# Performance work log

Hardware: AMD Instinct MI355X
Metric: run time of the kernel (lower is better)

## Reference

```python
import jax, jax.numpy as jnp
import numpy as np

N_NODES = 100000
N_EDGES = 1600000
N_FEAT = 256
HIDDEN = 128
N_CLASSES = 40


def gcn_conv(x, edge_index, W, b, num_nodes):
    # h = X W  (transform first, like torch_geometric GCNConv)
    h = x @ W  # [N, out]
    # add self loops
    loops = jnp.arange(num_nodes, dtype=edge_index.dtype)
    src = jnp.concatenate([edge_index[0], loops])
    dst = jnp.concatenate([edge_index[1], loops])
    # symmetric normalization: deg computed on dst (in-degree incl. self loop)
    deg = jax.ops.segment_sum(jnp.ones_like(dst, dtype=h.dtype), dst,
                              num_segments=num_nodes)
    dinv = jnp.where(deg > 0, jax.lax.rsqrt(deg), 0.0)
    norm = dinv[src] * dinv[dst]  # [E+N]
    # gather -> scale -> scatter-add
    msgs = h[src] * norm[:, None]
    out = jax.ops.segment_sum(msgs, dst, num_segments=num_nodes)
    return out + b


def setup_inputs() -> dict:
    key = jax.random.key(0)
    k1, k2, k3, k4, k5 = jax.random.split(key, 5)
    x = jax.random.normal(k1, (N_NODES, N_FEAT), dtype=jnp.float32)
    edge_index = jax.random.randint(k2, (2, N_EDGES), 0, N_NODES, dtype=jnp.int64)
    W1 = jax.random.normal(k3, (N_FEAT, HIDDEN), dtype=jnp.float32) * (1.0 / np.sqrt(N_FEAT))
    b1 = jnp.zeros((HIDDEN,), dtype=jnp.float32)
    W2 = jax.random.normal(k4, (HIDDEN, N_CLASSES), dtype=jnp.float32) * (1.0 / np.sqrt(HIDDEN))
    b2 = jnp.zeros((N_CLASSES,), dtype=jnp.float32)
    return {"x": x, "edge_index": edge_index, "W1": W1, "b1": b1, "W2": W2, "b2": b2}


def reference(x, edge_index, W1, b1, W2, b2):
    num_nodes = x.shape[0]
    h = gcn_conv(x, edge_index, W1, b1, num_nodes)
    h = jax.nn.relu(h)
    # dropout p=0.1 is identity in eval mode (self.training == False)
    out = gcn_conv(h, edge_index, W2, b2, num_nodes)
    return out
```

## Files before the change

### kernel.cpp

```cpp
#include <hip/hip_runtime.h>


#define NFEAT 256
#define HID   128
#define NCLS  40

__global__ void k_hist(const int* __restrict__ dst, int* __restrict__ deg, int E) {
    int stride = gridDim.x * blockDim.x;
    for (int e = blockIdx.x * blockDim.x + threadIdx.x; e < E; e += stride)
        atomicAdd(&deg[dst[e]], 1);
}

__global__ void k_scan1(const int* __restrict__ deg, int* __restrict__ rowptr,
                        int* __restrict__ blockSums, float* __restrict__ dinv, int N) {
    __shared__ int sums[256];
    int t = threadIdx.x;
    int base = blockIdx.x * 1024 + t * 4;
    int c[4];
#pragma unroll
    for (int j = 0; j < 4; j++) {
        int idx = base + j;
        c[j] = (idx < N) ? deg[idx] : 0;
        if (idx < N) dinv[idx] = rsqrtf((float)(c[j] + 1));
    }
    int s = c[0] + c[1] + c[2] + c[3];
    sums[t] = s;
    __syncthreads();
    for (int off = 1; off < 256; off <<= 1) {
        int v = (t >= off) ? sums[t - off] : 0;
        __syncthreads();
        sums[t] += v;
        __syncthreads();
    }
    int run = sums[t] - s;
#pragma unroll
    for (int j = 0; j < 4; j++) {
        int idx = base + j;
        if (idx < N) rowptr[idx] = run;
        run += c[j];
    }
    if (t == 255) blockSums[blockIdx.x] = sums[255];
}

__global__ void k_scan2(int* __restrict__ blockSums, int* __restrict__ rowptr,
                        int nblocks, int N) {
    __shared__ int sh[128];
    int t = threadIdx.x;
    int v = (t < nblocks) ? blockSums[t] : 0;
    sh[t] = v;
    __syncthreads();
    for (int off = 1; off < 128; off <<= 1) {
        int u = (t >= off) ? sh[t - off] : 0;
        __syncthreads();
        sh[t] += u;
        __syncthreads();
    }
    blockSums[t] = sh[t] - v;
    if (t == 127) rowptr[N] = sh[127];
}

__global__ void k_scan3(int* __restrict__ rowptr, const int* __restrict__ blockSums,
                        int* __restrict__ cursor, int N) {
    int stride = gridDim.x * blockDim.x;
    for (int i = blockIdx.x * blockDim.x + threadIdx.x; i < N; i += stride) {
        int v = rowptr[i] + blockSums[i >> 10];
        rowptr[i] = v;
        cursor[i] = v;
    }
}

__global__ void k_fill(const int* __restrict__ src, const int* __restrict__ dst,
                       int* __restrict__ cursor, int* __restrict__ col, int E) {
    int stride = gridDim.x * blockDim.x;
    for (int e = blockIdx.x * blockDim.x + threadIdx.x; e < E; e += stride) {
        int d = dst[e];
        int pos = atomicAdd(&cursor[d], 1);
        col[pos] = src[e];
    }
}

__global__ __launch_bounds__(256) void k_gemm1(const float* __restrict__ X,
                                               const float* __restrict__ W,
                                               const float* __restrict__ dinv,
                                               float* __restrict__ H, int M) {
    __shared__ float As[32][132];
    __shared__ float Bs[32][128];
    int t = threadIdx.x;
    int tx = t & 15, ty = t >> 4;
    int row0 = blockIdx.x * 128;

    float acc[8][8];
#pragma unroll
    for (int i = 0; i < 8; i++)
#pragma unroll
        for (int j = 0; j < 8; j++) acc[i][j] = 0.f;

    int arow = t >> 3;
    int acol = (t & 7) * 4;
    int brow = t >> 5;
    int bcol = (t & 31) * 4;

    for (int k0 = 0; k0 < NFEAT; k0 += 32) {
#pragma unroll
        for (int p = 0; p < 4; p++) {
            int r = p * 32 + arow;
            int gr = row0 + r;
            float4 v = make_float4(0.f, 0.f, 0.f, 0.f);
            if (gr < M) v = *(const float4*)&X[(size_t)gr * NFEAT + k0 + acol];
            As[acol + 0][r] = v.x; As[acol + 1][r] = v.y;
            As[acol + 2][r] = v.z; As[acol + 3][r] = v.w;
        }
#pragma unroll
        for (int p = 0; p < 4; p++) {
            int kr = p * 8 + brow;
            *(float4*)&Bs[kr][bcol] = *(const float4*)&W[(size_t)(k0 + kr) * HID + bcol];
        }
        __syncthreads();
#pragma unroll
        for (int kk = 0; kk < 32; kk++) {
            float a[8], b[8];
            *(float4*)&a[0] = *(const float4*)&As[kk][ty * 8];
            *(float4*)&a[4] = *(const float4*)&As[kk][ty * 8 + 4];
            *(float4*)&b[0] = *(const float4*)&Bs[kk][tx * 4];
            *(float4*)&b[4] = *(const float4*)&Bs[kk][64 + tx * 4];
#pragma unroll
            for (int i = 0; i < 8; i++)
#pragma unroll
                for (int j = 0; j < 8; j++) acc[i][j] += a[i] * b[j];
        }
        __syncthreads();
    }
#pragma unroll
    for (int i = 0; i < 8; i++) {
        int gr = row0 + ty * 8 + i;
        if (gr < M) {
            float dv = dinv[gr];
            float4 v0 = make_float4(acc[i][0] * dv, acc[i][1] * dv, acc[i][2] * dv, acc[i][3] * dv);
            float4 v1 = make_float4(acc[i][4] * dv, acc[i][5] * dv, acc[i][6] * dv, acc[i][7] * dv);
            *(float4*)&H[(size_t)gr * HID + tx * 4] = v0;
            *(float4*)&H[(size_t)gr * HID + 64 + tx * 4] = v1;
        }
    }
}

__global__ __launch_bounds__(256) void k_agg1(const float* __restrict__ H1,
                                              const int* __restrict__ rowptr,
                                              const int* __restrict__ col,
                                              const float* __restrict__ dinv,
                                              const float* __restrict__ b1,
                                              float* __restrict__ out, int N) {
    int node = blockIdx.x * 4 + (threadIdx.x >> 6);
    if (node >= N) return;
    int lane = threadIdx.x & 63;
    int g = lane >> 5;
    int c = lane & 31;

    float4 acc = make_float4(0.f, 0.f, 0.f, 0.f);
    if (g == 0)
        acc = *(const float4*)&H1[(size_t)node * HID + c * 4];

    int e = rowptr[node], e1 = rowptr[node + 1];
    for (; e + 7 < e1; e += 8) {
        int s0 = col[e + g];
        int s1 = col[e + 2 + g];
        int s2 = col[e + 4 + g];
        int s3 = col[e + 6 + g];
        float4 v0 = *(const float4*)&H1[(size_t)s0 * HID + c * 4];
        float4 v1 = *(const float4*)&H1[(size_t)s1 * HID + c * 4];
        float4 v2 = *(const float4*)&H1[(size_t)s2 * HID + c * 4];
        float4 v3 = *(const float4*)&H1[(size_t)s3 * HID + c * 4];
        acc.x += (v0.x + v1.x) + (v2.x + v3.x);
        acc.y += (v0.y + v1.y) + (v2.y + v3.y);
        acc.z += (v0.z + v1.z) + (v2.z + v3.z);
        acc.w += (v0.w + v1.w) + (v2.w + v3.w);
    }
    for (; e + 1 < e1; e += 2) {
        int s = col[e + g];
        float4 v = *(const float4*)&H1[(size_t)s * HID + c * 4];
        acc.x += v.x; acc.y += v.y; acc.z += v.z; acc.w += v.w;
    }
    if (e < e1 && g == 0) {
        int s = col[e];
        float4 v = *(const float4*)&H1[(size_t)s * HID + c * 4];
        acc.x += v.x; acc.y += v.y; acc.z += v.z; acc.w += v.w;
    }
    acc.x += __shfl_xor(acc.x, 32);
    acc.y += __shfl_xor(acc.y, 32);
    acc.z += __shfl_xor(acc.z, 32);
    acc.w += __shfl_xor(acc.w, 32);

    if (g == 0) {
        float dv = dinv[node];
        float4 bb = *(const float4*)&b1[c * 4];
        float4 r;
        r.x = fmaxf(acc.x * dv + bb.x, 0.f);
        r.y = fmaxf(acc.y * dv + bb.y, 0.f);
        r.z = fmaxf(acc.z * dv + bb.z, 0.f);
        r.w = fmaxf(acc.w * dv + bb.w, 0.f);
        *(float4*)&out[(size_t)node * HID + c * 4] = r;
    }
}

__global__ __launch_bounds__(256) void k_gemm2(const float* __restrict__ A,
                                               const float* __restrict__ W,
                                               const float* __restrict__ dinv,
                                               float* __restrict__ H, int M) {
    __shared__ float As[64][129];
    __shared__ float Ws[HID * NCLS];
    int t = threadIdx.x;
    for (int idx = t; idx < HID * NCLS; idx += 256) Ws[idx] = W[idx];

    int row0 = blockIdx.x * 64;
#pragma unroll
    for (int p = 0; p < 8; p++) {
        int flat = (p * 256 + t) * 4;
        int r = flat >> 7;
        int c = flat & 127;
        int gr = row0 + r;
        float4 v = make_float4(0.f, 0.f, 0.f, 0.f);
        if (gr < M) v = *(const float4*)&A[(size_t)gr * HID + c];
        As[r][c + 0] = v.x; As[r][c + 1] = v.y; As[r][c + 2] = v.z; As[r][c + 3] = v.w;
    }
    __syncthreads();

    int r = t >> 2;
    int cg = (t & 3) * 10;
    float acc[10];
#pragma unroll
    for (int j = 0; j < 10; j++) acc[j] = 0.f;
    for (int k = 0; k < HID; k++) {
        float a = As[r][k];
        const float* wrow = &Ws[k * NCLS + cg];
#pragma unroll
        for (int j = 0; j < 10; j++) acc[j] += a * wrow[j];
    }
    int gr = row0 + r;
    if (gr < M) {
        float dv = dinv[gr];
#pragma unroll
        for (int j = 0; j < 10; j++) H[(size_t)gr * NCLS + cg + j] = acc[j] * dv;
    }
}

__global__ __launch_bounds__(256) void k_agg2(const float* __restrict__ H2,
                                              const int* __restrict__ rowptr,
                                              const int* __restrict__ col,
                                              const float* __restrict__ dinv,
                                              const float* __restrict__ b2,
                                              float* __restrict__ out, int N) {
    int node = blockIdx.x * 4 + (threadIdx.x >> 6);
    if (node >= N) return;
    int lane = threadIdx.x & 63;
    int g = lane / 10;
    int c = lane % 10;
    bool active = g < 6;

    float4 acc = make_float4(0.f, 0.f, 0.f, 0.f);
    if (g == 0)
        acc = *(const float4*)&H2[(size_t)node * NCLS + c * 4];

    int e = rowptr[node], e1 = rowptr[node + 1];
    for (; e + 11 < e1; e += 12) {
        if (active) {
            int s0 = col[e + g];
            int s1 = col[e + 6 + g];
            float4 v0 = *(const float4*)&H2[(size_t)s0 * NCLS + c * 4];
            float4 v1 = *(const float4*)&H2[(size_t)s1 * NCLS + c * 4];
            acc.x += v0.x + v1.x;
            acc.y += v0.y + v1.y;
            acc.z += v0.z + v1.z;
            acc.w += v0.w + v1.w;
        }
    }
    for (; e < e1; e += 6) {
        int idx = e + g;
        if (active && idx < e1) {
            int s = col[idx];
            float4 v = *(const float4*)&H2[(size_t)s * NCLS + c * 4];
            acc.x += v.x; acc.y += v.y; acc.z += v.z; acc.w += v.w;
        }
    }
    float4 t1, t2;
    t1.x = __shfl(acc.x, lane + 30); t1.y = __shfl(acc.y, lane + 30);
    t1.z = __shfl(acc.z, lane + 30); t1.w = __shfl(acc.w, lane + 30);
    acc.x += t1.x; acc.y += t1.y; acc.z += t1.z; acc.w += t1.w;
    t1.x = __shfl(acc.x, lane + 10); t1.y = __shfl(acc.y, lane + 10);
    t1.z = __shfl(acc.z, lane + 10); t1.w = __shfl(acc.w, lane + 10);
    t2.x = __shfl(acc.x, lane + 20); t2.y = __shfl(acc.y, lane + 20);
    t2.z = __shfl(acc.z, lane + 20); t2.w = __shfl(acc.w, lane + 20);
    acc.x += t1.x + t2.x; acc.y += t1.y + t2.y;
    acc.z += t1.z + t2.z; acc.w += t1.w + t2.w;

    if (g == 0) {
        float dv = dinv[node];
        float4 bb = *(const float4*)&b2[c * 4];
        float4 r;
        r.x = acc.x * dv + bb.x;
        r.y = acc.y * dv + bb.y;
        r.z = acc.z * dv + bb.z;
        r.w = acc.w * dv + bb.w;
        *(float4*)&out[(size_t)node * NCLS + c * 4] = r;
    }
}

extern "C" void kernel_launch(void* const* d_in, const int* in_sizes, int n_in,
                              void* d_out, int out_size, void* d_ws, size_t ws_size,
                              hipStream_t stream) {
    const float* x  = (const float*)d_in[0];
    const int*   ei = (const int*)d_in[1];
    const float* W1 = (const float*)d_in[2];
    const float* b1 = (const float*)d_in[3];
    const float* W2 = (const float*)d_in[4];
    const float* b2 = (const float*)d_in[5];
    float* out = (float*)d_out;

    const int N = in_sizes[0] / NFEAT;
    const int E = in_sizes[1] / 2;
    const int* src = ei;
    const int* dst = ei + E;

    char* ws = (char*)d_ws;
    size_t off = 0;
    auto alloc = [&](size_t bytes) { size_t cur = off; off = (off + bytes + 255) & ~255ULL; return cur; };
    int*   deg       = (int*)(ws + alloc((size_t)N * 4));
    int*   rowptr    = (int*)(ws + alloc(((size_t)N + 1) * 4));
    int*   cursor    = (int*)(ws + alloc((size_t)N * 4));
    float* dinv      = (float*)(ws + alloc((size_t)N * 4));
    int*   blockSums = (int*)(ws + alloc(4096));
    int*   colv      = (int*)(ws + alloc((size_t)E * 4));
    float* h1s       = (float*)(ws + alloc((size_t)N * HID * 4));
    float* hrelu     = (float*)(ws + alloc((size_t)N * HID * 4));
    float* h2s       = h1s;

    hipMemsetAsync(deg, 0, (size_t)N * 4, stream);

    k_hist<<<2048, 256, 0, stream>>>(dst, deg, E);

    int nscan = (N + 1023) / 1024;
    k_scan1<<<nscan, 256, 0, stream>>>(deg, rowptr, blockSums, dinv, N);
    k_scan2<<<1, 128, 0, stream>>>(blockSums, rowptr, nscan, N);
    k_scan3<<<(N + 255) / 256, 256, 0, stream>>>(rowptr, blockSums, cursor, N);

    k_fill<<<4096, 256, 0, stream>>>(src, dst, cursor, colv, E);

    k_gemm1<<<(N + 127) / 128, 256, 0, stream>>>(x, W1, dinv, h1s, N);
    k_agg1<<<(N + 3) / 4, 256, 0, stream>>>(h1s, rowptr, colv, dinv, b1, hrelu, N);
    k_gemm2<<<(N + 63) / 64, 256, 0, stream>>>(hrelu, W2, dinv, h2s, N);
    k_agg2<<<(N + 3) / 4, 256, 0, stream>>>(h2s, rowptr, colv, dinv, b2, out, N);
}
```

Before: 655.8 us.

## Build CSR via two-level bucketed counting sort with shared-memory histograms

Replaces the per-node global atomic histogram, three-kernel scan and per-node atomic fill with a bucketed scheme. Nodes are grouped into buckets of 32. Bucket counts come from shared-memory histograms, edges are scattered into a staging buffer with per-bucket cursors, and each bucket's block then computes local degrees, rowptr, dinv and column placement in shared memory. This cuts global atomic contention and the number of kernel launches in CSR construction. In exchange it adds a packed staging pass, reused from the hrelu buffer, whose packing assumes source ids fit in 27 bits. It also relies on NB fitting in the fixed shared-memory histogram size.

After: 641.4 us. -2.2%, faster.

```diff
diff --git a/kernel.cpp b/kernel.cpp
--- a/kernel.cpp
+++ b/kernel.cpp
@@ -4,26 +4,37 @@
 #define NFEAT 256
 #define HID   128
 #define NCLS  40
-
-__global__ void k_hist(const int* __restrict__ dst, int* __restrict__ deg, int E) {
+#define NBMAX 3136
+
+__global__ __launch_bounds__(256) void kA_bhist(const int* __restrict__ dst,
+                                                int* __restrict__ bcount, int E, int NB) {
+    __shared__ int hist[NBMAX];
+    for (int i = threadIdx.x; i < NB; i += 256) hist[i] = 0;
+    __syncthreads();
     int stride = gridDim.x * blockDim.x;
     for (int e = blockIdx.x * blockDim.x + threadIdx.x; e < E; e += stride)
-        atomicAdd(&deg[dst[e]], 1);
-}
-
-__global__ void k_scan1(const int* __restrict__ deg, int* __restrict__ rowptr,
-                        int* __restrict__ blockSums, float* __restrict__ dinv, int N) {
+        atomicAdd(&hist[dst[e] >> 5], 1);
+    __syncthreads();
+    for (int i = threadIdx.x; i < NB; i += 256) {
+        int h = hist[i];
+        if (h) atomicAdd(&bcount[i], h);
+    }
+}
+
+__global__ __launch_bounds__(256) void kB_bscan(const int* __restrict__ bcount,
+                                                int* __restrict__ bstart,
+                                                int* __restrict__ bcursor,
+                                                int* __restrict__ rowptr,
+                                                int NB, int Nn, int E) {
     __shared__ int sums[256];
     int t = threadIdx.x;
-    int base = blockIdx.x * 1024 + t * 4;
-    int c[4];
-#pragma unroll
-    for (int j = 0; j < 4; j++) {
-        int idx = base + j;
-        c[j] = (idx < N) ? deg[idx] : 0;
-        if (idx < N) dinv[idx] = rsqrtf((float)(c[j] + 1));
-    }
-    int s = c[0] + c[1] + c[2] + c[3];
+    int per = (NB + 255) / 256;
+    int base = t * per;
+    int s = 0;
+    for (int j = 0; j < per; j++) {
+        int i = base + j;
+        if (i < NB) s += bcount[i];
+    }
     sums[t] = s;
     __syncthreads();
     for (int off = 1; off < 256; off <<= 1) {
@@ -33,49 +44,63 @@
         __syncthreads();
     }
     int run = sums[t] - s;
-#pragma unroll
-    for (int j = 0; j < 4; j++) {
-        int idx = base + j;
-        if (idx < N) rowptr[idx] = run;
-        run += c[j];
-    }
-    if (t == 255) blockSums[blockIdx.x] = sums[255];
-}
-
-__global__ void k_scan2(int* __restrict__ blockSums, int* __restrict__ rowptr,
-                        int nblocks, int N) {
-    __shared__ int sh[128];
-    int t = threadIdx.x;
-    int v = (t < nblocks) ? blockSums[t] : 0;
-    sh[t] = v;
-    __syncthreads();
-    for (int off = 1; off < 128; off <<= 1) {
-        int u = (t >= off) ? sh[t - off] : 0;
-        __syncthreads();
-        sh[t] += u;
-        __syncthreads();
-    }
-    blockSums[t] = sh[t] - v;
-    if (t == 127) rowptr[N] = sh[127];
-}
-
-__global__ void k_scan3(int* __restrict__ rowptr, const int* __restrict__ blockSums,
-                        int* __restrict__ cursor, int N) {
-    int stride = gridDim.x * blockDim.x;
-    for (int i = blockIdx.x * blockDim.x + threadIdx.x; i < N; i += stride) {
-        int v = rowptr[i] + blockSums[i >> 10];
-        rowptr[i] = v;
-        cursor[i] = v;
-    }
-}
-
-__global__ void k_fill(const int* __restrict__ src, const int* __restrict__ dst,
-                       int* __restrict__ cursor, int* __restrict__ col, int E) {
+    for (int j = 0; j < per; j++) {
+        int i = base + j;
+        if (i < NB) { bstart[i] = run; bcursor[i] = run; run += bcount[i]; }
+    }
+    if (t == 255) { bstart[NB] = run; rowptr[Nn] = E; }
+}
+
+__global__ __launch_bounds__(256) void kC_scatter(const int* __restrict__ src,
+                                                  const int* __restrict__ dst,
+                                                  int* __restrict__ bcursor,
+                                                  unsigned int* __restrict__ stage, int E) {
     int stride = gridDim.x * blockDim.x;
     for (int e = blockIdx.x * blockDim.x + threadIdx.x; e < E; e += stride) {
         int d = dst[e];
-        int pos = atomicAdd(&cursor[d], 1);
-        col[pos] = src[e];
+        int pos = atomicAdd(&bcursor[d >> 5], 1);
+        stage[pos] = (unsigned int)src[e] | ((unsigned int)(d & 31) << 27);
+    }
+}
+
+__global__ __launch_bounds__(256) void kD_fill(const unsigned int* __restrict__ stage,
+                                               const int* __restrict__ bstart,
+                                               int* __restrict__ rowptr,
+                                               float* __restrict__ dinv,
+                                               int* __restrict__ col, int Nn) {
+    __shared__ int deg32[32];
+    __shared__ int pref[32];
+    __shared__ int cur[32];
+    int b = blockIdx.x;
+    int t = threadIdx.x;
+    int bs = bstart[b], be = bstart[b + 1];
+    if (t < 32) deg32[t] = 0;
+    __syncthreads();
+    for (int i = bs + t; i < be; i += 256) {
+        unsigned int u = stage[i];
+        atomicAdd(&deg32[u >> 27], 1);
+    }
+    __syncthreads();
+    if (t == 0) {
+        int r = 0;
+        for (int j = 0; j < 32; j++) { pref[j] = r; r += deg32[j]; }
+    }
+    __syncthreads();
+    int n0 = b * 32;
+    if (t < 32) {
+        int n = n0 + t;
+        if (n < Nn) {
+            rowptr[n] = bs + pref[t];
+            dinv[n] = rsqrtf((float)(deg32[t] + 1));
+        }
+        cur[t] = pref[t];
+    }
+    __syncthreads();
+    for (int i = bs + t; i < be; i += 256) {
+        unsigned int u = stage[i];
+        int d = u >> 27;
+        int pos = bs + atomicAdd(&cur[d], 1);
+        col[pos] = (int)(u & 0x07FFFFFFu);
     }
 }
 
@@ -316,32 +341,30 @@
 
     const int N = in_sizes[0] / NFEAT;
     const int E = in_sizes[1] / 2;
+    const int NB = (N + 31) / 32;
     const int* src = ei;
     const int* dst = ei + E;
 
     char* ws = (char*)d_ws;
     size_t off = 0;
     auto alloc = [&](size_t bytes) { size_t cur = off; off = (off + bytes + 255) & ~255ULL; return cur; };
-    int*   deg       = (int*)(ws + alloc((size_t)N * 4));
-    int*   rowptr    = (int*)(ws + alloc(((size_t)N + 1) * 4));
-    int*   cursor    = (int*)(ws + alloc((size_t)N * 4));
-    float* dinv      = (float*)(ws + alloc((size_t)N * 4));
-    int*   blockSums = (int*)(ws + alloc(4096));
-    int*   colv      = (int*)(ws + alloc((size_t)E * 4));
-    float* h1s       = (float*)(ws + alloc((size_t)N * HID * 4));
-    float* hrelu     = (float*)(ws + alloc((size_t)N * HID * 4));
-    float* h2s       = h1s;
-
-    hipMemsetAsync(deg, 0, (size_t)N * 4, stream);
-
-    k_hist<<<2048, 256, 0, stream>>>(dst, deg, E);
-
-    int nscan = (N + 1023) / 1024;
-    k_scan1<<<nscan, 256, 0, stream>>>(deg, rowptr, blockSums, dinv, N);
-    k_scan2<<<1, 128, 0, stream>>>(blockSums, rowptr, nscan, N);
-    k_scan3<<<(N + 255) / 256, 256, 0, stream>>>(rowptr, blockSums, cursor, N);
-
-    k_fill<<<4096, 256, 0, stream>>>(src, dst, cursor, colv, E);
+    int*   rowptr  = (int*)(ws + alloc(((size_t)N + 1) * 4));
+    float* dinv    = (float*)(ws + alloc((size_t)N * 4));
+    int*   bcount  = (int*)(ws + alloc(((size_t)NB + 1) * 4));
+    int*   bstart  = (int*)(ws + alloc(((size_t)NB + 1) * 4));
+    int*   bcursor = (int*)(ws + alloc(((size_t)NB + 1) * 4));
+    int*   colv    = (int*)(ws + alloc((size_t)E * 4));
+    float* h1s     = (float*)(ws + alloc((size_t)N * HID * 4));
+    float* hrelu   = (float*)(ws + alloc((size_t)N * HID * 4));
+    float* h2s     = h1s;
+    unsigned int* stage = (unsigned int*)hrelu;
+
+    hipMemsetAsync(bcount, 0, ((size_t)NB + 1) * 4, stream);
+
+    kA_bhist<<<128, 256, 0, stream>>>(dst, bcount, E, NB);
+    kB_bscan<<<1, 256, 0, stream>>>(bcount, bstart, bcursor, rowptr, NB, N, E);
+    kC_scatter<<<2048, 256, 0, stream>>>(src, dst, bcursor, stage, E);
+    kD_fill<<<NB, 256, 0, stream>>>(stage, bstart, rowptr, dinv, colv, N);
 
     k_gemm1<<<(N + 127) / 128, 256, 0, stream>>>(x, W1, dinv, h1s, N);
     k_agg1<<<(N + 3) / 4, 256, 0, stream>>>(h1s, rowptr, colv, dinv, b1, hrelu, N);
```
